# Performance work log

Hardware: AMD Instinct MI355X
Metric: run time of the kernel (lower is better)

The kernel has to match this reference:

```python
import jax, jax.numpy as jnp
import numpy as np

FIXED_SIZE = 10
NUM_GRAPHS = 2000
NUM_PERM = 1


def setup_inputs() -> dict:
    key = jax.random.key(0)
    ks = jax.random.split(key, 8)
    N, E, D, H, O = 100000, 600000, 128, 256, 256
    x = jax.random.normal(ks[0], (N, D), dtype=jnp.float32)
    edge_index = jax.random.randint(ks[1], (2, E), 0, N)
    batch_ids = jnp.sort(jax.random.randint(ks[2], (N,), 0, NUM_GRAPHS))
    W1 = jax.random.normal(ks[3], (D + FIXED_SIZE, H), dtype=jnp.float32) * 0.05
    b1 = jnp.zeros((H,), dtype=jnp.float32)
    W2 = jax.random.normal(ks[4], (H, O), dtype=jnp.float32) * 0.05
    b2 = jnp.zeros((O,), dtype=jnp.float32)
    return {"x": x, "edge_index": edge_index, "batch_ids": batch_ids,
            "W1": W1, "b1": b1, "W2": W2, "b2": b2}


def _gnn(new_x, src, dst, W1, b1, W2, b2):
    # 2-layer GIN-style sum-aggregation node embedder
    N = new_x.shape[0]
    m = jax.ops.segment_sum(new_x[src], dst, num_segments=N)
    h = jax.nn.relu((new_x + m) @ W1 + b1)
    m = jax.ops.segment_sum(h[src], dst, num_segments=N)
    h = jax.nn.relu((h + m) @ W2 + b2)
    return h


def reference(x, edge_index, batch_ids, W1, b1, W2, b2):
    N = x.shape[0]
    src, dst = edge_index[0], edge_index[1]
    # segment starts (batch_ids is sorted)
    counts = jax.ops.segment_sum(jnp.ones((N,), jnp.int32), batch_ids, num_segments=NUM_GRAPHS)
    starts = jnp.cumsum(counts) - counts  # [G]
    perm_key = jax.random.key(42)
    out = None
    for p in range(NUM_PERM):
        # vectorized per-graph random permutation: sort random keys within each segment
        r = jax.random.uniform(jax.random.fold_in(perm_key, p), (N,))
        order = jnp.argsort(batch_ids.astype(jnp.float32) + r)  # groups by graph, random within
        # rank within graph after permutation (order preserves segment boundaries)
        ranks = jnp.zeros((N,), jnp.int32).at[order].set(
            jnp.arange(N, dtype=jnp.int32) - starts[batch_ids].astype(jnp.int32))
        # tiled eye(10) indexed by permuted position == one-hot of (rank % 10)
        ids = jax.nn.one_hot(ranks % FIXED_SIZE, FIXED_SIZE, dtype=x.dtype)
        new_x = jnp.concatenate([x, ids], axis=1)  # [N, D+10]
        h_v = _gnn(new_x, src, dst, W1, b1, W2, b2)
        h_g = jax.ops.segment_sum(h_v, batch_ids, num_segments=NUM_GRAPHS)  # global_add_pool
        contrib = h_g / NUM_PERM
        out = contrib if out is None else out + contrib
    return out
```

## Files before the change

### kernel.cpp

```cpp
#include <hip/hip_runtime.h>
#include <hip/hip_bf16.h>
#include <stdint.h>


#define D_IN   128
#define KRAW   138
#define K1     160
#define B1ROW  192
#define HDIM   256
#define NGRAPH 2000

typedef __bf16 bf16x8 __attribute__((ext_vector_type(8)));
typedef float  f32x4  __attribute__((ext_vector_type(4)));

__device__ __forceinline__ unsigned short f2b(float f) {
  __hip_bfloat16 h = __float2bfloat16(f);
  return __builtin_bit_cast(unsigned short, h);
}
__device__ __forceinline__ float blo(unsigned p) { return __uint_as_float(p << 16); }
__device__ __forceinline__ float bhi(unsigned p) { return __uint_as_float(p & 0xffff0000u); }

__device__ __forceinline__ void glds16(const unsigned short* g, unsigned short* l) {
  __builtin_amdgcn_global_load_lds(
      (const __attribute__((address_space(1))) unsigned int*)g,
      (__attribute__((address_space(3))) unsigned int*)l, 16, 0, 0);
}

__device__ __forceinline__ unsigned rotl32(unsigned x, int r) {
  return (x << r) | (x >> (32 - r));
}
__device__ __forceinline__ void threefry2x32(unsigned k0, unsigned k1,
                                             unsigned x0, unsigned x1,
                                             unsigned& o0, unsigned& o1) {
  unsigned ks2 = k0 ^ k1 ^ 0x1BD11BDAu;
  unsigned ks[3] = {k0, k1, ks2};
  x0 += ks[0]; x1 += ks[1];
  const int rotA[4] = {13, 15, 26, 6};
  const int rotB[4] = {17, 29, 16, 24};
#pragma unroll
  for (int i = 0; i < 5; ++i) {
    const int* rot = (i & 1) ? rotB : rotA;
#pragma unroll
    for (int j = 0; j < 4; ++j) {
      x0 += x1; x1 = rotl32(x1, rot[j]); x1 ^= x0;
    }
    x0 += ks[(i + 1) % 3];
    x1 += ks[(i + 2) % 3] + (unsigned)(i + 1);
  }
  o0 = x0; o1 = x1;
}

__global__ void k_prep2(const int* __restrict__ bids, const int* __restrict__ dst,
                        float* __restrict__ r, int* __restrict__ start,
                        int* __restrict__ cnt, int* __restrict__ deg, int N, int E) {
  int i = blockIdx.x * blockDim.x + threadIdx.x;
  if (i < E) atomicAdd(&deg[dst[i]], 1);
  if (i >= N) return;
  int half = N >> 1;
  if (i < half) {
    unsigned fk0, fk1;
    threefry2x32(0u, 42u, 0u, 0u, fk0, fk1);
    unsigned b0, b1v;
    threefry2x32(fk0, fk1, (unsigned)i, (unsigned)(i + half), b0, b1v);
    r[i]        = __uint_as_float((b0  >> 9) | 0x3f800000u) - 1.0f;
    r[i + half] = __uint_as_float((b1v >> 9) | 0x3f800000u) - 1.0f;
  }
  int g = bids[i];
  if (i == 0 || bids[i - 1] != g) start[g] = i;
  atomicAdd(&cnt[g], 1);
}

__global__ void k_rank(const float* __restrict__ r, const int* __restrict__ start,
                       const int* __restrict__ cnt, int* __restrict__ ids) {
  int g = blockIdx.x;
  int st = start[g], n = cnt[g];
  if (n <= 0) return;
  float gf = (float)g;
  for (int t = threadIdx.x; t < n; t += blockDim.x) {
    int v = st + t;
    float kv = gf + r[v];
    int c = 0;
    for (int u0 = 0; u0 < n; ++u0) {
      int u = st + u0;
      float ku = gf + r[u];
      c += (int)((ku < kv) | ((ku == kv) & (u < v)));
    }
    ids[v] = c % 10;
  }
}

__global__ void k_scan1(const int* __restrict__ deg, int* __restrict__ rowptr,
                        int* __restrict__ bsum, int N) {
  __shared__ int buf[256];
  int tid = threadIdx.x;
  int i = blockIdx.x * 256 + tid;
  int v = (i < N) ? deg[i] : 0;
  buf[tid] = v;
  __syncthreads();
  for (int off = 1; off < 256; off <<= 1) {
    int t = (tid >= off) ? buf[tid - off] : 0;
    __syncthreads();
    buf[tid] += t;
    __syncthreads();
  }
  if (i < N) rowptr[i] = buf[tid] - v;
  if (tid == 255) bsum[blockIdx.x] = buf[255];
}

__global__ void k_scan2(int* __restrict__ bsum, int nb) {
  __shared__ int buf[512];
  int tid = threadIdx.x;
  int v = (tid < nb) ? bsum[tid] : 0;
  buf[tid] = v;
  __syncthreads();
  for (int off = 1; off < 512; off <<= 1) {
    int t = (tid >= off) ? buf[tid - off] : 0;
    __syncthreads();
    buf[tid] += t;
    __syncthreads();
  }
  if (tid < nb) bsum[tid] = buf[tid] - v;
}

__global__ void k_scan3(int* __restrict__ rowptr, const int* __restrict__ bsum,
                        int N, int E) {
  int i = blockIdx.x * 256 + threadIdx.x;
  if (i < N) rowptr[i] += bsum[blockIdx.x];
  if (i == 0) rowptr[N] = E;
}

__global__ void k_scatter(const int* __restrict__ src, const int* __restrict__ dst,
                          const int* __restrict__ rowptr, int* __restrict__ fill,
                          int* __restrict__ csr, int E) {
  int e = blockIdx.x * 256 + threadIdx.x;
  if (e >= E) return;
  int d = dst[e];
  int pos = rowptr[d] + atomicAdd(&fill[d], 1);
  csr[pos] = src[e];
}

__global__ void k_pre(const float* __restrict__ x, const float* __restrict__ W1,
                      const float* __restrict__ W2, unsigned short* __restrict__ xb,
                      unsigned short* __restrict__ Wpt, unsigned short* __restrict__ W2t,
                      int n8, int xbb) {
  int bid = blockIdx.x;
  int tid = threadIdx.x;
  if (bid < xbb) {
    int i = bid * 256 + tid;
    if (i >= n8) return;
    const float4* xp = reinterpret_cast<const float4*>(x) + (size_t)i * 2;
    float4 v0 = xp[0], v1 = xp[1];
    uint4 o;
    o.x = (unsigned)f2b(v0.x) | ((unsigned)f2b(v0.y) << 16);
    o.y = (unsigned)f2b(v0.z) | ((unsigned)f2b(v0.w) << 16);
    o.z = (unsigned)f2b(v1.x) | ((unsigned)f2b(v1.y) << 16);
    o.w = (unsigned)f2b(v1.z) | ((unsigned)f2b(v1.w) << 16);
    reinterpret_cast<uint4*>(xb)[i] = o;
  } else {
    int j = (bid - xbb) * 256 + tid;
    if (j < HDIM * B1ROW) {
      int n = j / B1ROW, k = j % B1ROW;
      Wpt[j] = f2b(k < KRAW ? W1[k * HDIM + n] : 0.f);
    } else {
      int j2 = j - HDIM * B1ROW;
      if (j2 < HDIM * HDIM) {
        int n = j2 >> 8, k = j2 & 255;
        W2t[j2] = f2b(W2[k * HDIM + n]);
      }
    }
  }
}

__global__ void k_agg1(const unsigned short* __restrict__ xb, const int* __restrict__ ids,
                       const int* __restrict__ rowptr, const int* __restrict__ csr,
                       unsigned short* __restrict__ agg1, int N) {
  int v = blockIdx.x * 4 + (threadIdx.x >> 6);
  if (v >= N) return;
  int l = threadIdx.x & 63;
  const unsigned* xbase = reinterpret_cast<const unsigned*>(xb);
  unsigned sv = xbase[(size_t)v * 64 + l];
  float a0 = blo(sv), a1 = bhi(sv);
  int e0 = rowptr[v], e1 = rowptr[v + 1];
  int e = e0;
  for (; e + 4 <= e1; e += 4) {
    int u0 = csr[e], u1 = csr[e + 1], u2 = csr[e + 2], u3 = csr[e + 3];
    unsigned t0 = xbase[(size_t)u0 * 64 + l];
    unsigned t1 = xbase[(size_t)u1 * 64 + l];
    unsigned t2 = xbase[(size_t)u2 * 64 + l];
    unsigned t3 = xbase[(size_t)u3 * 64 + l];
    a0 += blo(t0) + blo(t1) + blo(t2) + blo(t3);
    a1 += bhi(t0) + bhi(t1) + bhi(t2) + bhi(t3);
  }
  for (; e < e1; ++e) {
    unsigned t = xbase[(size_t)csr[e] * 64 + l];
    a0 += blo(t); a1 += bhi(t);
  }
  int cnt10[10] = {};
  for (int base = e0; base < e1; base += 64) {
    int ee = base + l;
    int id = (ee < e1) ? ids[csr[ee]] : -1;
#pragma unroll
    for (int k = 0; k < 10; ++k)
      cnt10[k] += (int)__popcll(__ballot(id == k));
  }
  int myid = ids[v];
  unsigned* row32 = reinterpret_cast<unsigned*>(agg1 + (size_t)v * K1);
  row32[l] = (unsigned)f2b(a0) | ((unsigned)f2b(a1) << 16);
  if (l < 16) {
    float v0 = 0.f, v1 = 0.f;
#pragma unroll
    for (int kk = 0; kk < 10; ++kk) {
      float cv = (float)(cnt10[kk] + (myid == kk ? 1 : 0));
      if (2 * l == kk) v0 = cv;
      if (2 * l + 1 == kk) v1 = cv;
    }
    row32[64 + l] = (unsigned)f2b(v0) | ((unsigned)f2b(v1) << 16);
  }
}

__global__ void k_agg2(const unsigned short* __restrict__ h,
                       const int* __restrict__ rowptr, const int* __restrict__ csr,
                       unsigned short* __restrict__ hs, int N) {
  int v = blockIdx.x * 4 + (threadIdx.x >> 6);
  if (v >= N) return;
  int l = threadIdx.x & 63;
  const uint2* base = reinterpret_cast<const uint2*>(h);
  uint2 t = base[(size_t)v * 64 + l];
  float a0 = blo(t.x), a1 = bhi(t.x), a2 = blo(t.y), a3 = bhi(t.y);
  int e0 = rowptr[v], e1 = rowptr[v + 1];
  int e = e0;
  for (; e + 4 <= e1; e += 4) {
    int u0 = csr[e], u1 = csr[e + 1], u2 = csr[e + 2], u3 = csr[e + 3];
    uint2 s0 = base[(size_t)u0 * 64 + l];
    uint2 s1 = base[(size_t)u1 * 64 + l];
    uint2 s2 = base[(size_t)u2 * 64 + l];
    uint2 s3 = base[(size_t)u3 * 64 + l];
    a0 += blo(s0.x) + blo(s1.x) + blo(s2.x) + blo(s3.x);
    a1 += bhi(s0.x) + bhi(s1.x) + bhi(s2.x) + bhi(s3.x);
    a2 += blo(s0.y) + blo(s1.y) + blo(s2.y) + blo(s3.y);
    a3 += bhi(s0.y) + bhi(s1.y) + bhi(s2.y) + bhi(s3.y);
  }
  for (; e < e1; ++e) {
    uint2 s = base[(size_t)csr[e] * 64 + l];
    a0 += blo(s.x); a1 += bhi(s.x); a2 += blo(s.y); a3 += bhi(s.y);
  }
  uint2 o;
  o.x = (unsigned)f2b(a0) | ((unsigned)f2b(a1) << 16);
  o.y = (unsigned)f2b(a2) | ((unsigned)f2b(a3) << 16);
  reinterpret_cast<uint2*>(hs)[(size_t)v * 64 + l] = o;
}

template <int KT, int BROW, int NT, bool POOL>
__global__ __launch_bounds__(512, 1) void k_gemm(
    const unsigned short* __restrict__ A, const unsigned short* __restrict__ Bt,
    const float* __restrict__ bias, unsigned short* __restrict__ H,
    const int* __restrict__ bids, float* __restrict__ out, int M) {
  constexpr int ROWB = BROW * 2;
  __shared__ __align__(16) unsigned short b_s[HDIM * BROW];
  __shared__ __align__(16) unsigned short a_s[3 * 4096];
  __shared__ int seg_l[POOL ? 128 : 1];
  __shared__ int gseg_l[POOL ? 128 : 1];
  __shared__ int wtot[2];
  __shared__ int nseg_sh;

  const int tid = threadIdx.x;
  const int w = tid >> 6, l = tid & 63;
  const int wm = w >> 2, wn = w & 3;
  const int lr = l & 15, lq = l >> 4, lk = lq * 8;
  const int b = blockIdx.x;
  const int TT = (M + 127) >> 7;
  const int ntb = (TT > b) ? ((TT - b + 255) >> 8) : 0;
  const int total = ntb * NT;

  constexpr int BITERS = BROW / 16;
#pragma unroll
  for (int it = 0; it < BITERS; ++it) {
    int d = (it * 512 + tid) * 16;
    int n = d / ROWB;
    int inrow = d - n * ROWB;
    int u = inrow ^ ((n & 7) << 4);
    glds16(Bt + (size_t)n * BROW + (u >> 1), b_s + (size_t)(it * 512 + w * 64) * 8);
  }
  auto stageA = [&](int s) {
    int buf = s - (s / 3) * 3;
    int m0 = (b + (s / NT) * 256) << 7;
    int k0 = (s % NT) * 32;
    int d = tid * 16;
    int u = d ^ (((d >> 7) & 7) << 4);
    int r = ((u >> 7) << 1) | ((u >> 6) & 1);
    int k = (u >> 1) & 31;
    glds16(A + (size_t)(m0 + r) * KT + k0 + k, a_s + buf * 4096 + w * 512);
  };
  if (total > 0) stageA(0);
  if (total > 1) stageA(1);
  if (total > 1) { asm volatile("s_waitcnt vmcnt(1)" ::: "memory"); }
  else           { asm volatile("s_waitcnt vmcnt(0)" ::: "memory"); }
  __builtin_amdgcn_s_barrier();
  __builtin_amdgcn_sched_barrier(0);

  float bv[4];
#pragma unroll
  for (int nf = 0; nf < 4; ++nf) bv[nf] = bias[wn * 64 + nf * 16 + lr];

  int aoff[4];
#pragma unroll
  for (int mf = 0; mf < 4; ++mf) {
    int R = wm * 64 + mf * 16 + lr;
    aoff[mf] = (((R >> 1) * 128 + (R & 1) * 64 + lk * 2) ^ (((R >> 1) & 7) << 4));
  }

  int s = 0;
  for (int ti = 0; ti < ntb; ++ti) {
    const int m0t = (b + ti * 256) << 7;
    f32x4 acc[4][4] = {};
    for (int ks = 0; ks < NT; ++ks, ++s) {
      const bool pre = (s + 2 < total);
      if (pre) stageA(s + 2);
      const char* ab = reinterpret_cast<const char*>(a_s) + (s - (s / 3) * 3) * 8192;
      bf16x8 af[4], bfr[4];
#pragma unroll
      for (int mf = 0; mf < 4; ++mf)
        af[mf] = *reinterpret_cast<const bf16x8*>(ab + aoff[mf]);
#pragma unroll
      for (int nf = 0; nf < 4; ++nf) {
        int n = wn * 64 + nf * 16 + lr;
        int bb = n * ROWB + (((ks * 32 + lk) * 2) ^ ((n & 7) << 4));
        bfr[nf] = *reinterpret_cast<const bf16x8*>(reinterpret_cast<const char*>(b_s) + bb);
      }
      __builtin_amdgcn_s_setprio(1);
#pragma unroll
      for (int mf = 0; mf < 4; ++mf)
#pragma unroll
        for (int nf = 0; nf < 4; ++nf)
          acc[mf][nf] = __builtin_amdgcn_mfma_f32_16x16x32_bf16(af[mf], bfr[nf], acc[mf][nf], 0, 0, 0);
      __builtin_amdgcn_s_setprio(0);
      if (pre) { asm volatile("s_waitcnt vmcnt(1)" ::: "memory"); }
      else     { asm volatile("s_waitcnt vmcnt(0)" ::: "memory"); }
      __builtin_amdgcn_s_barrier();
      __builtin_amdgcn_sched_barrier(0);
    }

    if constexpr (!POOL) {
#pragma unroll
      for (int mf = 0; mf < 4; ++mf)
#pragma unroll
        for (int q = 0; q < 4; ++q) {
          int grow = m0t + wm * 64 + mf * 16 + lq * 4 + q;
          if (grow < M) {
            size_t ro = (size_t)grow * HDIM + wn * 64 + lr;
#pragma unroll
            for (int nf = 0; nf < 4; ++nf) {
              float vv = acc[mf][nf][q] + bv[nf];
              H[ro + nf * 16] = f2b(vv > 0.f ? vv : 0.f);
            }
          }
        }
    } else {
      if (tid < 128) {
        int i0 = m0t + tid; i0 = i0 < M ? i0 : M - 1;
        int i1 = m0t + tid - 1; i1 = i1 < M ? i1 : M - 1; i1 = i1 > 0 ? i1 : 0;
        int g = bids[i0];
        bool bnd = (tid > 0) && (g != bids[i1]);
        unsigned long long mb = __ballot(bnd);
        int lane = tid & 63;
        int incl = (int)__popcll(mb & (~0ULL >> (63 - lane)));
        seg_l[tid] = incl;
        if (lane == 63) wtot[tid >> 6] = incl;
      }
      asm volatile("s_waitcnt lgkmcnt(0)" ::: "memory");
      __builtin_amdgcn_s_barrier();
      __builtin_amdgcn_sched_barrier(0);
      if (tid < 128) {
        int sfin = seg_l[tid] + ((tid >= 64) ? wtot[0] : 0);
        seg_l[tid] = sfin;
        int i0 = m0t + tid; i0 = i0 < M ? i0 : M - 1;
        int i1 = m0t + tid - 1; i1 = i1 < M ? i1 : M - 1; i1 = i1 > 0 ? i1 : 0;
        int g = bids[i0];
        if (tid == 0 || g != bids[i1]) gseg_l[sfin] = g;
        if (tid == 127) nseg_sh = sfin + 1;
      }
      asm volatile("s_waitcnt lgkmcnt(0)" ::: "memory");
      __builtin_amdgcn_s_barrier();
      __builtin_amdgcn_sched_barrier(0);
#pragma unroll
      for (int mf = 0; mf < 4; ++mf)
#pragma unroll
        for (int nf = 0; nf < 4; ++nf)
#pragma unroll
          for (int q = 0; q < 4; ++q) {
            float vv = acc[mf][nf][q] + bv[nf];
            acc[mf][nf][q] = vv > 0.f ? vv : 0.f;
          }
      int msg[16];
      bool mok[16];
#pragma unroll
      for (int mf = 0; mf < 4; ++mf)
#pragma unroll
        for (int q = 0; q < 4; ++q) {
          int R = wm * 64 + mf * 16 + lq * 4 + q;
          msg[mf * 4 + q] = seg_l[R];
          mok[mf * 4 + q] = (m0t + R) < M;
        }
      int nseg = nseg_sh;
      for (int sg = 0; sg < nseg; ++sg) {
        float v0 = 0.f, v1 = 0.f, v2 = 0.f, v3 = 0.f;
#pragma unroll
        for (int mf = 0; mf < 4; ++mf)
#pragma unroll
          for (int q = 0; q < 4; ++q) {
            if ((msg[mf * 4 + q] == sg) & mok[mf * 4 + q]) {
              v0 += acc[mf][0][q]; v1 += acc[mf][1][q];
              v2 += acc[mf][2][q]; v3 += acc[mf][3][q];
            }
          }
        v0 += __shfl_xor(v0, 16); v0 += __shfl_xor(v0, 32);
        v1 += __shfl_xor(v1, 16); v1 += __shfl_xor(v1, 32);
        v2 += __shfl_xor(v2, 16); v2 += __shfl_xor(v2, 32);
        v3 += __shfl_xor(v3, 16); v3 += __shfl_xor(v3, 32);
        if (lq == 0) {
          float* op = out + (size_t)gseg_l[sg] * HDIM + wn * 64 + lr;
          atomicAdd(&op[0],  v0);
          atomicAdd(&op[16], v1);
          atomicAdd(&op[32], v2);
          atomicAdd(&op[48], v3);
        }
      }
      __builtin_amdgcn_s_barrier();
      __builtin_amdgcn_sched_barrier(0);
    }
  }
}

extern "C" void kernel_launch(void* const* d_in, const int* in_sizes, int n_in,
                              void* d_out, int out_size, void* d_ws, size_t ws_size,
                              hipStream_t stream) {
  const float* x    = (const float*)d_in[0];
  const int*   ei   = (const int*)d_in[1];
  const int*   bids = (const int*)d_in[2];
  const float* W1   = (const float*)d_in[3];
  const float* b1   = (const float*)d_in[4];
  const float* W2   = (const float*)d_in[5];
  const float* b2   = (const float*)d_in[6];
  float* out = (float*)d_out;

  const int N = in_sizes[2];
  const int E = in_sizes[1] / 2;
  const int* src = ei;
  const int* dst = ei + E;

  char* ws = (char*)d_ws;
  size_t off = 0;
  auto alloc = [&](size_t bytes) {
    size_t o = off;
    off = (off + bytes + 255) & ~(size_t)255;
    return o;
  };
  float* r      = (float*)(ws + alloc((size_t)N * 4));
  int*   ids    = (int*)(ws + alloc((size_t)N * 4));
  int*   start  = (int*)(ws + alloc((size_t)NGRAPH * 4));
  int*   cnt    = (int*)(ws + alloc((size_t)NGRAPH * 4));
  int*   deg    = (int*)(ws + alloc((size_t)N * 4));
  int*   fill   = (int*)(ws + alloc((size_t)N * 4));
  int*   rowptr = (int*)(ws + alloc((size_t)(N + 1) * 4));
  int*   bsum   = (int*)(ws + alloc(512 * 4));
  int*   csr    = (int*)(ws + alloc((size_t)E * 4));
  unsigned short* Wpt  = (unsigned short*)(ws + alloc((size_t)HDIM * B1ROW * 2));
  unsigned short* W2t  = (unsigned short*)(ws + alloc((size_t)HDIM * HDIM * 2));
  unsigned short* xb   = (unsigned short*)(ws + alloc((size_t)N * D_IN * 2));
  unsigned short* agg1 = (unsigned short*)(ws + alloc((size_t)(N + 128) * K1 * 2));
  unsigned short* h    = (unsigned short*)(ws + alloc((size_t)(N + 128) * HDIM * 2));
  unsigned short* hsum = (unsigned short*)(ws + alloc((size_t)(N + 128) * HDIM * 2));
  (void)ws_size;

  size_t zspan = (size_t)((char*)(fill + N) - (char*)cnt);
  hipMemsetAsync(cnt, 0, zspan, stream);
  hipMemsetAsync(out, 0, (size_t)out_size * 4, stream);

  const int nb = (N + 255) / 256;
  const int n8 = N * 16;
  const int xbb = (n8 + 255) / 256;
  const int wb = (HDIM * B1ROW + HDIM * HDIM + 255) / 256;

  k_prep2<<<(E + 255) / 256, 256, 0, stream>>>(bids, dst, r, start, cnt, deg, N, E);
  k_pre<<<xbb + wb, 256, 0, stream>>>(x, W1, W2, xb, Wpt, W2t, n8, xbb);
  k_scan1<<<nb, 256, 0, stream>>>(deg, rowptr, bsum, N);
  k_scan2<<<1, 512, 0, stream>>>(bsum, nb);
  k_scan3<<<nb, 256, 0, stream>>>(rowptr, bsum, N, E);
  k_scatter<<<(E + 255) / 256, 256, 0, stream>>>(src, dst, rowptr, fill, csr, E);
  k_rank<<<NGRAPH, 64, 0, stream>>>(r, start, cnt, ids);
  k_agg1<<<(N + 3) / 4, 256, 0, stream>>>(xb, ids, rowptr, csr, agg1, N);

  k_gemm<K1, B1ROW, 5, false><<<256, 512, 0, stream>>>(agg1, Wpt, b1, h, nullptr, nullptr, N);

  k_agg2<<<(N + 3) / 4, 256, 0, stream>>>(h, rowptr, csr, hsum, N);

  k_gemm<HDIM, HDIM, 8, true><<<256, 512, 0, stream>>>(hsum, W2t, b2, nullptr, bids, out, N);
}
```

Measured before the change: 371.6 us.

## Reorder second layer as transform-then-aggregate with FP8 gather and fused pooling

Uses linearity, (h+A h)W2 = hW2 + A(hW2), to run the second GEMM before aggregation. The GEMM output is stored as 8-bit E4M3-like floats, and a new kernel gathers neighbours, adds bias, applies ReLU and pools per graph through shared-memory reductions. The input features are also stored in 8-bit for the first aggregation, which halves gather bytes. This cuts memory traffic in both gather phases and removes the separate hsum buffer, at the cost of precision from 8-bit storage of activations and inputs.

```diff
diff --git a/kernel.cpp b/kernel.cpp
--- a/kernel.cpp
+++ b/kernel.cpp
@@ -9,6 +9,7 @@
 #define B1ROW  192
 #define HDIM   256
 #define NGRAPH 2000
+#define MAXS   6
 
 typedef __bf16 bf16x8 __attribute__((ext_vector_type(8)));
 typedef float  f32x4  __attribute__((ext_vector_type(4)));
@@ -19,6 +20,24 @@
 }
 __device__ __forceinline__ float blo(unsigned p) { return __uint_as_float(p << 16); }
 __device__ __forceinline__ float bhi(unsigned p) { return __uint_as_float(p & 0xffff0000u); }
+
+__device__ __forceinline__ unsigned e8(float f) {
+  unsigned u = __float_as_uint(f);
+  unsigned s = (u >> 24) & 0x80u;
+  float a = fabsf(f);
+  if (!(a >= 0.015625f)) return s;
+  a = fminf(a, 448.f);
+  unsigned b = __float_as_uint(a);
+  b += 0x0007FFFFu + ((b >> 20) & 1u);
+  unsigned e = (b >> 23) - 120u;
+  unsigned m = (b >> 20) & 7u;
+  return s | (e << 3) | m;
+}
+__device__ __forceinline__ float d8(unsigned byte) {
+  unsigned m = byte & 0x7fu;
+  unsigned bits = (0x3C000000u + (m << 20)) | ((byte & 0x80u) << 24);
+  return m ? __uint_as_float(bits) : 0.f;
+}
 
 __device__ __forceinline__ void glds16(const unsigned short* g, unsigned short* l) {
   __builtin_amdgcn_global_load_lds(
@@ -140,7 +159,7 @@
 }
 
 __global__ void k_pre(const float* __restrict__ x, const float* __restrict__ W1,
-                      const float* __restrict__ W2, unsigned short* __restrict__ xb,
+                      const float* __restrict__ W2, unsigned char* __restrict__ x8,
                       unsigned short* __restrict__ Wpt, unsigned short* __restrict__ W2t,
                       int n8, int xbb) {
   int bid = blockIdx.x;
@@ -150,12 +169,10 @@
     if (i >= n8) return;
     const float4* xp = reinterpret_cast<const float4*>(x) + (size_t)i * 2;
     float4 v0 = xp[0], v1 = xp[1];
-    uint4 o;
-    o.x = (unsigned)f2b(v0.x) | ((unsigned)f2b(v0.y) << 16);
-    o.y = (unsigned)f2b(v0.z) | ((unsigned)f2b(v0.w) << 16);
-    o.z = (unsigned)f2b(v1.x) | ((unsigned)f2b(v1.y) << 16);
-    o.w = (unsigned)f2b(v1.z) | ((unsigned)f2b(v1.w) << 16);
-    reinterpret_cast<uint4*>(xb)[i] = o;
+    uint2 o;
+    o.x = e8(v0.x) | (e8(v0.y) << 8) | (e8(v0.z) << 16) | (e8(v0.w) << 24);
+    o.y = e8(v1.x) | (e8(v1.y) << 8) | (e8(v1.z) << 16) | (e8(v1.w) << 24);
+    reinterpret_cast<uint2*>(x8)[i] = o;
   } else {
     int j = (bid - xbb) * 256 + tid;
     if (j < HDIM * B1ROW) {
@@ -171,29 +188,28 @@
   }
 }
 
-__global__ void k_agg1(const unsigned short* __restrict__ xb, const int* __restrict__ ids,
+__global__ void k_agg1(const unsigned char* __restrict__ x8, const int* __restrict__ ids,
                        const int* __restrict__ rowptr, const int* __restrict__ csr,
                        unsigned short* __restrict__ agg1, int N) {
   int v = blockIdx.x * 4 + (threadIdx.x >> 6);
   if (v >= N) return;
   int l = threadIdx.x & 63;
-  const unsigned* xbase = reinterpret_cast<const unsigned*>(xb);
-  unsigned sv = xbase[(size_t)v * 64 + l];
-  float a0 = blo(sv), a1 = bhi(sv);
+  const unsigned short* xbase = reinterpret_cast<const unsigned short*>(x8);
+  unsigned t = xbase[(size_t)v * 64 + l];
+  float a0 = d8(t & 0xffu), a1 = d8(t >> 8);
   int e0 = rowptr[v], e1 = rowptr[v + 1];
   int e = e0;
   for (; e + 4 <= e1; e += 4) {
-    int u0 = csr[e], u1 = csr[e + 1], u2 = csr[e + 2], u3 = csr[e + 3];
-    unsigned t0 = xbase[(size_t)u0 * 64 + l];
-    unsigned t1 = xbase[(size_t)u1 * 64 + l];
-    unsigned t2 = xbase[(size_t)u2 * 64 + l];
-    unsigned t3 = xbase[(size_t)u3 * 64 + l];
-    a0 += blo(t0) + blo(t1) + blo(t2) + blo(t3);
-    a1 += bhi(t0) + bhi(t1) + bhi(t2) + bhi(t3);
+    unsigned t0 = xbase[(size_t)csr[e] * 64 + l];
+    unsigned t1 = xbase[(size_t)csr[e + 1] * 64 + l];
+    unsigned t2 = xbase[(size_t)csr[e + 2] * 64 + l];
+    unsigned t3 = xbase[(size_t)csr[e + 3] * 64 + l];
+    a0 += d8(t0 & 0xffu) + d8(t1 & 0xffu) + d8(t2 & 0xffu) + d8(t3 & 0xffu);
+    a1 += d8(t0 >> 8) + d8(t1 >> 8) + d8(t2 >> 8) + d8(t3 >> 8);
   }
   for (; e < e1; ++e) {
-    unsigned t = xbase[(size_t)csr[e] * 64 + l];
-    a0 += blo(t); a1 += bhi(t);
+    unsigned tt = xbase[(size_t)csr[e] * 64 + l];
+    a0 += d8(tt & 0xffu); a1 += d8(tt >> 8);
   }
   int cnt10[10] = {};
   for (int base = e0; base < e1; base += 64) {
@@ -218,50 +234,13 @@
   }
 }
 
-__global__ void k_agg2(const unsigned short* __restrict__ h,
-                       const int* __restrict__ rowptr, const int* __restrict__ csr,
-                       unsigned short* __restrict__ hs, int N) {
-  int v = blockIdx.x * 4 + (threadIdx.x >> 6);
-  if (v >= N) return;
-  int l = threadIdx.x & 63;
-  const uint2* base = reinterpret_cast<const uint2*>(h);
-  uint2 t = base[(size_t)v * 64 + l];
-  float a0 = blo(t.x), a1 = bhi(t.x), a2 = blo(t.y), a3 = bhi(t.y);
-  int e0 = rowptr[v], e1 = rowptr[v + 1];
-  int e = e0;
-  for (; e + 4 <= e1; e += 4) {
-    int u0 = csr[e], u1 = csr[e + 1], u2 = csr[e + 2], u3 = csr[e + 3];
-    uint2 s0 = base[(size_t)u0 * 64 + l];
-    uint2 s1 = base[(size_t)u1 * 64 + l];
-    uint2 s2 = base[(size_t)u2 * 64 + l];
-    uint2 s3 = base[(size_t)u3 * 64 + l];
-    a0 += blo(s0.x) + blo(s1.x) + blo(s2.x) + blo(s3.x);
-    a1 += bhi(s0.x) + bhi(s1.x) + bhi(s2.x) + bhi(s3.x);
-    a2 += blo(s0.y) + blo(s1.y) + blo(s2.y) + blo(s3.y);
-    a3 += bhi(s0.y) + bhi(s1.y) + bhi(s2.y) + bhi(s3.y);
-  }
-  for (; e < e1; ++e) {
-    uint2 s = base[(size_t)csr[e] * 64 + l];
-    a0 += blo(s.x); a1 += bhi(s.x); a2 += blo(s.y); a3 += bhi(s.y);
-  }
-  uint2 o;
-  o.x = (unsigned)f2b(a0) | ((unsigned)f2b(a1) << 16);
-  o.y = (unsigned)f2b(a2) | ((unsigned)f2b(a3) << 16);
-  reinterpret_cast<uint2*>(hs)[(size_t)v * 64 + l] = o;
-}
-
-template <int KT, int BROW, int NT, bool POOL>
+template <int KT, int BROW, int NT, int EPI>
 __global__ __launch_bounds__(512, 1) void k_gemm(
     const unsigned short* __restrict__ A, const unsigned short* __restrict__ Bt,
-    const float* __restrict__ bias, unsigned short* __restrict__ H,
-    const int* __restrict__ bids, float* __restrict__ out, int M) {
+    const float* __restrict__ bias, void* __restrict__ Hout, int M) {
   constexpr int ROWB = BROW * 2;
   __shared__ __align__(16) unsigned short b_s[HDIM * BROW];
   __shared__ __align__(16) unsigned short a_s[3 * 4096];
-  __shared__ int seg_l[POOL ? 128 : 1];
-  __shared__ int gseg_l[POOL ? 128 : 1];
-  __shared__ int wtot[2];
-  __shared__ int nseg_sh;
 
   const int tid = threadIdx.x;
   const int w = tid >> 6, l = tid & 63;
@@ -299,8 +278,10 @@
   __builtin_amdgcn_sched_barrier(0);
 
   float bv[4];
-#pragma unroll
-  for (int nf = 0; nf < 4; ++nf) bv[nf] = bias[wn * 64 + nf * 16 + lr];
+  if constexpr (EPI == 0) {
+#pragma unroll
+    for (int nf = 0; nf < 4; ++nf) bv[nf] = bias[wn * 64 + nf * 16 + lr];
+  }
 
   int aoff[4];
 #pragma unroll
@@ -340,93 +321,133 @@
       __builtin_amdgcn_sched_barrier(0);
     }
 
-    if constexpr (!POOL) {
-#pragma unroll
-      for (int mf = 0; mf < 4; ++mf)
-#pragma unroll
-        for (int q = 0; q < 4; ++q) {
-          int grow = m0t + wm * 64 + mf * 16 + lq * 4 + q;
-          if (grow < M) {
-            size_t ro = (size_t)grow * HDIM + wn * 64 + lr;
+#pragma unroll
+    for (int mf = 0; mf < 4; ++mf)
+#pragma unroll
+      for (int q = 0; q < 4; ++q) {
+        int grow = m0t + wm * 64 + mf * 16 + lq * 4 + q;
+        if (grow < M) {
+          size_t ro = (size_t)grow * HDIM + wn * 64 + lr;
+          if constexpr (EPI == 0) {
+            unsigned short* H = (unsigned short*)Hout;
 #pragma unroll
             for (int nf = 0; nf < 4; ++nf) {
               float vv = acc[mf][nf][q] + bv[nf];
               H[ro + nf * 16] = f2b(vv > 0.f ? vv : 0.f);
             }
+          } else {
+            unsigned char* H8 = (unsigned char*)Hout;
+#pragma unroll
+            for (int nf = 0; nf < 4; ++nf)
+              H8[ro + nf * 16] = (unsigned char)e8(acc[mf][nf][q]);
           }
         }
+      }
+  }
+}
+
+__global__ __launch_bounds__(256) void k_gp(
+    const unsigned char* __restrict__ y8, const int* __restrict__ bids,
+    const int* __restrict__ rowptr, const int* __restrict__ csr,
+    const float* __restrict__ b2, float* __restrict__ out, int N) {
+  __shared__ float red[4][MAXS][HDIM];
+  __shared__ int seg_l[128];
+  __shared__ int gseg_l[128];
+  __shared__ int wtot2[2];
+  __shared__ int nseg_sh;
+  const int tid = threadIdx.x;
+  const int w = tid >> 6, l = tid & 63;
+  const int v0 = blockIdx.x * 128;
+
+  float* rz = &red[0][0][0];
+  for (int i = tid; i < 4 * MAXS * HDIM; i += 256) rz[i] = 0.f;
+
+  if (tid < 128) {
+    int i0 = v0 + tid; i0 = i0 < N ? i0 : N - 1;
+    int i1 = v0 + tid - 1; i1 = i1 < N ? i1 : N - 1; i1 = i1 > 0 ? i1 : 0;
+    int g = bids[i0];
+    bool bnd = (tid > 0) && (g != bids[i1]);
+    unsigned long long mb = __ballot(bnd);
+    int lane = tid & 63;
+    int incl = (int)__popcll(mb & (~0ULL >> (63 - lane)));
+    seg_l[tid] = incl;
+    if (lane == 63) wtot2[tid >> 6] = incl;
+  }
+  __syncthreads();
+  if (tid < 128) {
+    int sfin = seg_l[tid] + ((tid >= 64) ? wtot2[0] : 0);
+    seg_l[tid] = sfin;
+    int i0 = v0 + tid; i0 = i0 < N ? i0 : N - 1;
+    int i1 = v0 + tid - 1; i1 = i1 < N ? i1 : N - 1; i1 = i1 > 0 ? i1 : 0;
+    int g = bids[i0];
+    if (tid == 0 || g != bids[i1]) gseg_l[sfin] = g;
+    if (tid == 127) nseg_sh = sfin + 1;
+  }
+  __syncthreads();
+  const int nseg = nseg_sh;
+  const bool fb = (nseg > MAXS);
+
+  float bv0 = b2[l * 4 + 0], bv1 = b2[l * 4 + 1];
+  float bv2 = b2[l * 4 + 2], bv3 = b2[l * 4 + 3];
+  const unsigned* yb = reinterpret_cast<const unsigned*>(y8);
+
+  float a0 = 0.f, a1 = 0.f, a2 = 0.f, a3 = 0.f;
+  int cur = seg_l[w * 32];
+  for (int i = 0; i < 32; ++i) {
+    int idx = w * 32 + i;
+    int v = v0 + idx;
+    if (v >= N) break;
+    int sg = seg_l[idx];
+    if (sg != cur) {
+      if (!fb) {
+        float* rp = &red[w][cur][l * 4];
+        rp[0] += a0; rp[1] += a1; rp[2] += a2; rp[3] += a3;
+      }
+      a0 = a1 = a2 = a3 = 0.f;
+      cur = sg;
+    }
+    unsigned t = yb[(size_t)v * 64 + l];
+    float s0 = d8(t & 0xffu), s1 = d8((t >> 8) & 0xffu);
+    float s2 = d8((t >> 16) & 0xffu), s3 = d8(t >> 24);
+    int e0 = rowptr[v], e1 = rowptr[v + 1];
+    int e = e0;
+    for (; e + 4 <= e1; e += 4) {
+      unsigned t0 = yb[(size_t)csr[e] * 64 + l];
+      unsigned t1 = yb[(size_t)csr[e + 1] * 64 + l];
+      unsigned t2 = yb[(size_t)csr[e + 2] * 64 + l];
+      unsigned t3 = yb[(size_t)csr[e + 3] * 64 + l];
+      s0 += d8(t0 & 0xffu) + d8(t1 & 0xffu) + d8(t2 & 0xffu) + d8(t3 & 0xffu);
+      s1 += d8((t0 >> 8) & 0xffu) + d8((t1 >> 8) & 0xffu) + d8((t2 >> 8) & 0xffu) + d8((t3 >> 8) & 0xffu);
+      s2 += d8((t0 >> 16) & 0xffu) + d8((t1 >> 16) & 0xffu) + d8((t2 >> 16) & 0xffu) + d8((t3 >> 16) & 0xffu);
+      s3 += d8(t0 >> 24) + d8(t1 >> 24) + d8(t2 >> 24) + d8(t3 >> 24);
+    }
+    for (; e < e1; ++e) {
+      unsigned tt = yb[(size_t)csr[e] * 64 + l];
+      s0 += d8(tt & 0xffu); s1 += d8((tt >> 8) & 0xffu);
+      s2 += d8((tt >> 16) & 0xffu); s3 += d8(tt >> 24);
+    }
+    s0 = fmaxf(s0 + bv0, 0.f); s1 = fmaxf(s1 + bv1, 0.f);
+    s2 = fmaxf(s2 + bv2, 0.f); s3 = fmaxf(s3 + bv3, 0.f);
+    if (fb) {
+      int g = bids[v];
+      float* op = out + (size_t)g * HDIM + l * 4;
+      if (s0 > 0.f) atomicAdd(&op[0], s0);
+      if (s1 > 0.f) atomicAdd(&op[1], s1);
+      if (s2 > 0.f) atomicAdd(&op[2], s2);
+      if (s3 > 0.f) atomicAdd(&op[3], s3);
     } else {
-      if (tid < 128) {
-        int i0 = m0t + tid; i0 = i0 < M ? i0 : M - 1;
-        int i1 = m0t + tid - 1; i1 = i1 < M ? i1 : M - 1; i1 = i1 > 0 ? i1 : 0;
-        int g = bids[i0];
-        bool bnd = (tid > 0) && (g != bids[i1]);
-        unsigned long long mb = __ballot(bnd);
-        int lane = tid & 63;
-        int incl = (int)__popcll(mb & (~0ULL >> (63 - lane)));
-        seg_l[tid] = incl;
-        if (lane == 63) wtot[tid >> 6] = incl;
-      }
-      asm volatile("s_waitcnt lgkmcnt(0)" ::: "memory");
-      __builtin_amdgcn_s_barrier();
-      __builtin_amdgcn_sched_barrier(0);
-      if (tid < 128) {
-        int sfin = seg_l[tid] + ((tid >= 64) ? wtot[0] : 0);
-        seg_l[tid] = sfin;
-        int i0 = m0t + tid; i0 = i0 < M ? i0 : M - 1;
-        int i1 = m0t + tid - 1; i1 = i1 < M ? i1 : M - 1; i1 = i1 > 0 ? i1 : 0;
-        int g = bids[i0];
-        if (tid == 0 || g != bids[i1]) gseg_l[sfin] = g;
-        if (tid == 127) nseg_sh = sfin + 1;
-      }
-      asm volatile("s_waitcnt lgkmcnt(0)" ::: "memory");
-      __builtin_amdgcn_s_barrier();
-      __builtin_amdgcn_sched_barrier(0);
-#pragma unroll
-      for (int mf = 0; mf < 4; ++mf)
-#pragma unroll
-        for (int nf = 0; nf < 4; ++nf)
-#pragma unroll
-          for (int q = 0; q < 4; ++q) {
-            float vv = acc[mf][nf][q] + bv[nf];
-            acc[mf][nf][q] = vv > 0.f ? vv : 0.f;
-          }
-      int msg[16];
-      bool mok[16];
-#pragma unroll
-      for (int mf = 0; mf < 4; ++mf)
-#pragma unroll
-        for (int q = 0; q < 4; ++q) {
-          int R = wm * 64 + mf * 16 + lq * 4 + q;
-          msg[mf * 4 + q] = seg_l[R];
-          mok[mf * 4 + q] = (m0t + R) < M;
-        }
-      int nseg = nseg_sh;
-      for (int sg = 0; sg < nseg; ++sg) {
-        float v0 = 0.f, v1 = 0.f, v2 = 0.f, v3 = 0.f;
-#pragma unroll
-        for (int mf = 0; mf < 4; ++mf)
-#pragma unroll
-          for (int q = 0; q < 4; ++q) {
-            if ((msg[mf * 4 + q] == sg) & mok[mf * 4 + q]) {
-              v0 += acc[mf][0][q]; v1 += acc[mf][1][q];
-              v2 += acc[mf][2][q]; v3 += acc[mf][3][q];
-            }
-          }
-        v0 += __shfl_xor(v0, 16); v0 += __shfl_xor(v0, 32);
-        v1 += __shfl_xor(v1, 16); v1 += __shfl_xor(v1, 32);
-        v2 += __shfl_xor(v2, 16); v2 += __shfl_xor(v2, 32);
-        v3 += __shfl_xor(v3, 16); v3 += __shfl_xor(v3, 32);
-        if (lq == 0) {
-          float* op = out + (size_t)gseg_l[sg] * HDIM + wn * 64 + lr;
-          atomicAdd(&op[0],  v0);
-          atomicAdd(&op[16], v1);
-          atomicAdd(&op[32], v2);
-          atomicAdd(&op[48], v3);
-        }
-      }
-      __builtin_amdgcn_s_barrier();
-      __builtin_amdgcn_sched_barrier(0);
+      a0 += s0; a1 += s1; a2 += s2; a3 += s3;
+    }
+  }
+  if (!fb) {
+    float* rp = &red[w][cur][l * 4];
+    rp[0] += a0; rp[1] += a1; rp[2] += a2; rp[3] += a3;
+  }
+  __syncthreads();
+  if (!fb) {
+    for (int sg = 0; sg < nseg; ++sg) {
+      float val = red[0][sg][tid] + red[1][sg][tid] + red[2][sg][tid] + red[3][sg][tid];
+      if (val != 0.f) atomicAdd(&out[(size_t)gseg_l[sg] * HDIM + tid], val);
     }
   }
 }
@@ -464,12 +485,12 @@
   int*   rowptr = (int*)(ws + alloc((size_t)(N + 1) * 4));
   int*   bsum   = (int*)(ws + alloc(512 * 4));
   int*   csr    = (int*)(ws + alloc((size_t)E * 4));
-  unsigned short* Wpt  = (unsigned short*)(ws + alloc((size_t)HDIM * B1ROW * 2));
-  unsigned short* W2t  = (unsigned short*)(ws + alloc((size_t)HDIM * HDIM * 2));
-  unsigned short* xb   = (unsigned short*)(ws + alloc((size_t)N * D_IN * 2));
+  unsigned short* Wpt = (unsigned short*)(ws + alloc((size_t)HDIM * B1ROW * 2));
+  unsigned short* W2t = (unsigned short*)(ws + alloc((size_t)HDIM * HDIM * 2));
+  unsigned char*  x8  = (unsigned char*)(ws + alloc((size_t)N * D_IN));
   unsigned short* agg1 = (unsigned short*)(ws + alloc((size_t)(N + 128) * K1 * 2));
   unsigned short* h    = (unsigned short*)(ws + alloc((size_t)(N + 128) * HDIM * 2));
-  unsigned short* hsum = (unsigned short*)(ws + alloc((size_t)(N + 128) * HDIM * 2));
+  unsigned char*  y8   = (unsigned char*)(ws + alloc((size_t)(N + 128) * HDIM));
   (void)ws_size;
 
   size_t zspan = (size_t)((char*)(fill + N) - (char*)cnt);
@@ -482,17 +503,16 @@
   const int wb = (HDIM * B1ROW + HDIM * HDIM + 255) / 256;
 
   k_prep2<<<(E + 255) / 256, 256, 0, stream>>>(bids, dst, r, start, cnt, deg, N, E);
-  k_pre<<<xbb + wb, 256, 0, stream>>>(x, W1, W2, xb, Wpt, W2t, n8, xbb);
+  k_pre<<<xbb + wb, 256, 0, stream>>>(x, W1, W2, x8, Wpt, W2t, n8, xbb);
   k_scan1<<<nb, 256, 0, stream>>>(deg, rowptr, bsum, N);
   k_scan2<<<1, 512, 0, stream>>>(bsum, nb);
   k_scan3<<<nb, 256, 0, stream>>>(rowptr, bsum, N, E);
   k_scatter<<<(E + 255) / 256, 256, 0, stream>>>(src, dst, rowptr, fill, csr, E);
   k_rank<<<NGRAPH, 64, 0, stream>>>(r, start, cnt, ids);
-  k_agg1<<<(N + 3) / 4, 256, 0, stream>>>(xb, ids, rowptr, csr, agg1, N);
-
-  k_gemm<K1, B1ROW, 5, false><<<256, 512, 0, stream>>>(agg1, Wpt, b1, h, nullptr, nullptr, N);
-
-  k_agg2<<<(N + 3) / 4, 256, 0, stream>>>(h, rowptr, csr, hsum, N);
-
-  k_gemm<HDIM, HDIM, 8, true><<<256, 512, 0, stream>>>(hsum, W2t, b2, nullptr, bids, out, N);
-}
+  k_agg1<<<(N + 3) / 4, 256, 0, stream>>>(x8, ids, rowptr, csr, agg1, N);
+
+  k_gemm<K1, B1ROW, 5, 0><<<256, 512, 0, stream>>>(agg1, Wpt, b1, (void*)h, N);
+  k_gemm<HDIM, HDIM, 8, 1><<<256, 512, 0, stream>>>(h, W2t, nullptr, (void*)y8, N);
+
+  k_gp<<<(N + 127) / 128, 256, 0, stream>>>(y8, bids, rowptr, csr, b2, out, N);
+}
```

Result: slower. 423.7 us (+14.0%).
